# Performance work log

Hardware: AMD Instinct MI355X
Metric: run time of the kernel (lower is better)

## Reference

```python
import jax, jax.numpy as jnp
import numpy as np

B, D, M, C = 8192, 2048, 8, 1000

def setup_inputs() -> dict:
    key = jax.random.key(0)
    k1, k2, k3, k4, k5 = jax.random.split(key, 5)
    scale = 1.0 / np.sqrt(D)
    return {
        "x": jax.random.normal(k1, (B, D), dtype=jnp.float32),
        "model_weights": jax.random.normal(k2, (M, D, C), dtype=jnp.float32) * scale,
        "model_bias": jax.random.normal(k3, (M, C), dtype=jnp.float32) * 0.01,
        "resnet_weight": jax.random.normal(k4, (D, M * C), dtype=jnp.float32) * scale,
        "resnet_bias": jax.random.normal(k5, (M * C,), dtype=jnp.float32) * 0.01,
    }

def reference(x, model_weights, model_bias, resnet_weight, resnet_bias):
    # Per-submodel logits: [B, M, C]
    outputs = jnp.einsum("bd,mdc->bmc", x, model_weights) + model_bias[None, :, :]
    # Fusion weights from the weighting network: [B, M, C]
    w = (x @ resnet_weight + resnet_bias).reshape(x.shape[0], model_weights.shape[0], model_weights.shape[2])
    # Fused weighted sum over models (replaces the triple Python loop): [B, C]
    result = jnp.sum(outputs * w, axis=1)
    return result
```

## Files before the change

### kernel.cpp

```cpp
#include <hip/hip_runtime.h>
#include <hip/hip_bf16.h>
#include <stdint.h>

#define BDIM 8192
#define DDIM 2048
#define MDIM 8
#define CDIM 1000
#define CPAD 1024
#define NPAD 8192

typedef __attribute__((ext_vector_type(8))) short bf16x8;
typedef __attribute__((ext_vector_type(4))) float f32x4;

__device__ __forceinline__ unsigned short f2bf(float f) {
    union { float f; unsigned u; } v; v.f = f;
    unsigned r = v.u + 0x7fffu + ((v.u >> 16) & 1u);
    return (unsigned short)(r >> 16);
}

__device__ __forceinline__ void gl_lds16(const void* g, void* l) {
    __builtin_amdgcn_global_load_lds(
        (const __attribute__((address_space(1))) void*)g,
        (__attribute__((address_space(3))) void*)l,
        16, 0, 0);
}

__global__ void cast_x_kernel(const float4* __restrict__ x, ushort* __restrict__ xb) {
    int i = blockIdx.x * blockDim.x + threadIdx.x;
    float4 v = x[i];
    ushort4 o;
    o.x = f2bf(v.x); o.y = f2bf(v.y); o.z = f2bf(v.z); o.w = f2bf(v.w);
    *(ushort4*)&xb[(size_t)i * 4] = o;
}

__global__ void prep_w(const float* __restrict__ MW, ushort* __restrict__ wb) {
    __shared__ float tile[32][33];
    int m  = blockIdx.z;
    int c0 = blockIdx.x * 32;
    int d0 = blockIdx.y * 32;
    int tx = threadIdx.x, ty = threadIdx.y;
    const float* src = MW + (size_t)m * DDIM * CDIM;
#pragma unroll
    for (int i = 0; i < 4; i++) {
        int d = d0 + ty + i * 8;
        int c = c0 + tx;
        tile[ty + i * 8][tx] = (c < CDIM) ? src[(size_t)d * CDIM + c] : 0.f;
    }
    __syncthreads();
#pragma unroll
    for (int i = 0; i < 4; i++) {
        int c = c0 + ty + i * 8;
        int d = d0 + tx;
        wb[(size_t)(c * 8 + m) * DDIM + d] = f2bf(tile[tx][ty + i * 8]);
    }
}

__global__ void prep_r(const float* __restrict__ R, ushort* __restrict__ rb) {
    __shared__ float tile[32][33];
    int m  = blockIdx.z;
    int c0 = blockIdx.x * 32;
    int d0 = blockIdx.y * 32;
    int tx = threadIdx.x, ty = threadIdx.y;
#pragma unroll
    for (int i = 0; i < 4; i++) {
        int d = d0 + ty + i * 8;
        int c = c0 + tx;
        tile[ty + i * 8][tx] = (c < CDIM) ? R[(size_t)d * (MDIM * CDIM) + m * CDIM + c] : 0.f;
    }
    __syncthreads();
#pragma unroll
    for (int i = 0; i < 4; i++) {
        int c = c0 + ty + i * 8;
        int d = d0 + tx;
        rb[(size_t)(c * 8 + m) * DDIM + d] = f2bf(tile[tx][ty + i * 8]);
    }
}

__global__ void prep_bias(const float* __restrict__ mb, const float* __restrict__ rbv,
                          float* __restrict__ mb2, float* __restrict__ rb2) {
    int n = blockIdx.x * 256 + threadIdx.x;
    int c = n >> 3, m = n & 7;
    mb2[n] = (c < CDIM) ? mb[m * CDIM + c] : 0.f;
    rb2[n] = (c < CDIM) ? rbv[m * CDIM + c] : 0.f;
}

#define BM 256
#define BN 128
#define BK 32
#define NT (DDIM / BK)


#define STAGE_A(G, L) do {                                                     \
    _Pragma("unroll")                                                          \
    for (int it_ = 0; it_ < 2; ++it_) {                                        \
        int ci_ = it_ * 512 + tid;                                             \
        int r_ = ci_ >> 2, cc_ = ci_ & 3;                                      \
        gl_lds16((G) + (size_t)r_ * DDIM + (size_t)((cc_ ^ ((r_ >> 1) & 3)) << 3), \
                 (L) + (size_t)(it_ * 512 + wbase) * 8);                       \
    }                                                                          \
} while (0)

#define STAGE_B(G, L) do {                                                     \
    int r_ = tid >> 2, cc_ = tid & 3;                                          \
    gl_lds16((G) + (size_t)r_ * DDIM + (size_t)((cc_ ^ ((r_ >> 1) & 3)) << 3), \
             (L) + (size_t)wbase * 8);                                         \
} while (0)

#define LDA4(AC, H) do {                                                       \
    _Pragma("unroll")                                                          \
    for (int i_ = 0; i_ < 4; i_++) {                                           \
        int row_ = wm * 128 + (H) * 64 + i_ * 16 + (lane & 15);                \
        int cc_ = lane >> 4;                                                   \
        af[i_] = *(const bf16x8*)&(AC)[row_ * BK + ((cc_ ^ ((row_ >> 1) & 3)) << 3)]; \
    }                                                                          \
} while (0)

#define LDB2(BS, BF) do {                                                      \
    _Pragma("unroll")                                                          \
    for (int j_ = 0; j_ < 2; j_++) {                                           \
        int row_ = wn * 32 + j_ * 16 + (lane & 15);                            \
        int cc_ = lane >> 4;                                                   \
        BF[j_] = *(const bf16x8*)&(BS)[row_ * BK + ((cc_ ^ ((row_ >> 1) & 3)) << 3)]; \
    }                                                                          \
} while (0)

#define MM16(H) do {                                                           \
    __builtin_amdgcn_s_setprio(1);                                             \
    _Pragma("unroll")                                                          \
    for (int i_ = 0; i_ < 4; i_++)                                             \
    _Pragma("unroll")                                                          \
    for (int j_ = 0; j_ < 2; j_++) {                                           \
        acc1[(H) * 4 + i_][j_] = __builtin_amdgcn_mfma_f32_16x16x32_bf16(      \
            af[i_], bf1[j_], acc1[(H) * 4 + i_][j_], 0, 0, 0);                 \
        acc2[(H) * 4 + i_][j_] = __builtin_amdgcn_mfma_f32_16x16x32_bf16(      \
            af[i_], bf2[j_], acc2[(H) * 4 + i_][j_], 0, 0, 0);                 \
    }                                                                          \
    __builtin_amdgcn_s_setprio(0);                                             \
} while (0)

#define FENCE() asm volatile("" ::: "memory")
#define BARRIER() do { FENCE(); __builtin_amdgcn_s_barrier(); FENCE(); } while (0)
#define WAITV(N) asm volatile("s_waitcnt vmcnt(" #N ")" ::: "memory")

__global__ __launch_bounds__(512, 2) void gemm_fused(
    const ushort* __restrict__ xb, const ushort* __restrict__ wb,
    const ushort* __restrict__ rb,
    const float* __restrict__ mb2, const float* __restrict__ rb2,
    float* __restrict__ out) {
    __shared__ ushort As[2][BM * BK];
    __shared__ ushort B1s[2][BN * BK];
    __shared__ ushort B2s[2][BN * BK];

    int tid   = threadIdx.x;
    int lane  = tid & 63;
    int wid   = tid >> 6;
    int wm    = wid >> 2;
    int wn    = wid & 3;
    int wbase = tid & ~63;

    int wg = blockIdx.x;
    int wgs = (wg & 7) * 256 + (wg >> 3);
    int tile_m = wgs >> 6;
    int tile_n = wgs & 63;
    int brow = tile_m * BM;
    int bn0  = tile_n * BN;

    const ushort* xg  = xb + (size_t)brow * DDIM;
    const ushort* w1g = wb + (size_t)bn0 * DDIM;
    const ushort* w2g = rb + (size_t)bn0 * DDIM;

    f32x4 acc1[8][2] = {};
    f32x4 acc2[8][2] = {};
    bf16x8 af[4], bf1[2], bf2[2];

    STAGE_A(xg,        As[0]);
    STAGE_B(w1g,       B1s[0]);
    STAGE_B(w2g,       B2s[0]);
    STAGE_A(xg + BK,   As[1]);
    WAITV(2);
    BARRIER();

#pragma unroll 2
    for (int t = 0; t < NT; ++t) {
        int buf = t & 1;
        ushort* Ac  = As[buf];
        ushort* B1c = B1s[buf];
        ushort* B2c = B2s[buf];
        ushort* B1n = B1s[buf ^ 1];
        ushort* B2n = B2s[buf ^ 1];
        const int kn  = (t + 1) * BK;
        const int kn2 = (t + 2) * BK;

        LDA4(Ac, 0);
        LDB2(B1c, bf1);
        LDB2(B2c, bf2);
        STAGE_B(w1g + kn, B1n);
        STAGE_B(w2g + kn, B2n);
        BARRIER();
        MM16(0);
        BARRIER();

        LDA4(Ac, 1);
        STAGE_A(xg + kn2, Ac);
        BARRIER();
        MM16(1);
        WAITV(2);
        BARRIER();
    }
    WAITV(0);

#pragma unroll
    for (int j = 0; j < 2; j++) {
        int np = bn0 + wn * 32 + j * 16 + (lane & 15);
        float bb1 = mb2[np];
        float bb2 = rb2[np];
        int c = tile_n * 16 + wn * 4 + j * 2 + ((lane >> 3) & 1);
#pragma unroll
        for (int rf = 0; rf < 8; rf++) {
#pragma unroll
            for (int r = 0; r < 4; r++) {
                float p = (acc1[rf][j][r] + bb1) * (acc2[rf][j][r] + bb2);
                p += __shfl_xor(p, 1);
                p += __shfl_xor(p, 2);
                p += __shfl_xor(p, 4);
                if ((lane & 7) == 0 && c < CDIM) {
                    int row = brow + wm * 128 + rf * 16 + ((lane >> 4) << 2) + r;
                    out[(size_t)row * CDIM + c] = p;
                }
            }
        }
    }
}

extern "C" void kernel_launch(void* const* d_in, const int* in_sizes, int n_in,
                              void* d_out, int out_size, void* d_ws, size_t ws_size,
                              hipStream_t stream) {
    const float* x   = (const float*)d_in[0];
    const float* mw  = (const float*)d_in[1];
    const float* mb  = (const float*)d_in[2];
    const float* rw  = (const float*)d_in[3];
    const float* rbv = (const float*)d_in[4];
    float* out = (float*)d_out;

    char* ws = (char*)d_ws;
    ushort* xb  = (ushort*)ws;
    ushort* wb  = (ushort*)(ws + (size_t)33554432);
    ushort* rb  = (ushort*)(ws + (size_t)67108864);
    float*  mb2 = (float*)(ws + (size_t)100663296);
    float*  rb2 = (float*)(ws + (size_t)100696064);

    cast_x_kernel<<<BDIM * DDIM / (256 * 4), 256, 0, stream>>>((const float4*)x, xb);
    prep_w<<<dim3(CPAD / 32, DDIM / 32, MDIM), dim3(32, 8), 0, stream>>>(mw, wb);
    prep_r<<<dim3(CPAD / 32, DDIM / 32, MDIM), dim3(32, 8), 0, stream>>>(rw, rb);
    prep_bias<<<NPAD / 256, 256, 0, stream>>>(mb, rbv, mb2, rb2);

    gemm_fused<<<dim3((BDIM / BM) * (NPAD / BN)), 512, 0, stream>>>(xb, wb, rb, mb2, rb2, out);
}
```

Before: 641.7 us.

## Shrink GEMM tile to 128x128 with 4 waves and triple-buffered A staging

Halves the row tile to 128 and the workgroup to 256 threads (4 waves, each owning all 128 rows and a 32-column slice). A is now staged into a 3-deep LDS ring and B into double buffers, all prefetched two K-steps ahead, so every stage load is issued after the current buffer's reads. This aims for deeper prefetch and more, smaller workgroups for better latency hiding. In exchange each tile reuses x and the weights less, which raises total global and LDS traffic per FLOP, and the loop is no longer unrolled.

```diff
diff --git a/kernel.cpp b/kernel.cpp
--- a/kernel.cpp
+++ b/kernel.cpp
@@ -84,34 +84,27 @@
     rb2[n] = (c < CDIM) ? rbv[m * CDIM + c] : 0.f;
 }
 
-#define BM 256
+#define BM 128
 #define BN 128
 #define BK 32
 #define NT (DDIM / BK)
 
-
-#define STAGE_A(G, L) do {                                                     \
+#define STAGE(G, L) do {                                                       \
     _Pragma("unroll")                                                          \
     for (int it_ = 0; it_ < 2; ++it_) {                                        \
-        int ci_ = it_ * 512 + tid;                                             \
+        int ci_ = it_ * 256 + tid;                                             \
         int r_ = ci_ >> 2, cc_ = ci_ & 3;                                      \
         gl_lds16((G) + (size_t)r_ * DDIM + (size_t)((cc_ ^ ((r_ >> 1) & 3)) << 3), \
-                 (L) + (size_t)(it_ * 512 + wbase) * 8);                       \
-    }                                                                          \
-} while (0)
-
-#define STAGE_B(G, L) do {                                                     \
-    int r_ = tid >> 2, cc_ = tid & 3;                                          \
-    gl_lds16((G) + (size_t)r_ * DDIM + (size_t)((cc_ ^ ((r_ >> 1) & 3)) << 3), \
-             (L) + (size_t)wbase * 8);                                         \
-} while (0)
-
-#define LDA4(AC, H) do {                                                       \
+                 (L) + (size_t)(it_ * 256 + wbase) * 8);                       \
+    }                                                                          \
+} while (0)
+
+#define LDA4(AC, I0) do {                                                      \
     _Pragma("unroll")                                                          \
     for (int i_ = 0; i_ < 4; i_++) {                                           \
-        int row_ = wm * 128 + (H) * 64 + i_ * 16 + (lane & 15);                \
+        int row_ = ((I0) + i_) * 16 + (lane & 15);                             \
         int cc_ = lane >> 4;                                                   \
-        af[i_] = *(const bf16x8*)&(AC)[row_ * BK + ((cc_ ^ ((row_ >> 1) & 3)) << 3)]; \
+        af[(I0) + i_] = *(const bf16x8*)&(AC)[row_ * BK + ((cc_ ^ ((row_ >> 1) & 3)) << 3)]; \
     }                                                                          \
 } while (0)
 
@@ -124,16 +117,16 @@
     }                                                                          \
 } while (0)
 
-#define MM16(H) do {                                                           \
+#define MM16(I0) do {                                                          \
     __builtin_amdgcn_s_setprio(1);                                             \
     _Pragma("unroll")                                                          \
     for (int i_ = 0; i_ < 4; i_++)                                             \
     _Pragma("unroll")                                                          \
     for (int j_ = 0; j_ < 2; j_++) {                                           \
-        acc1[(H) * 4 + i_][j_] = __builtin_amdgcn_mfma_f32_16x16x32_bf16(      \
-            af[i_], bf1[j_], acc1[(H) * 4 + i_][j_], 0, 0, 0);                 \
-        acc2[(H) * 4 + i_][j_] = __builtin_amdgcn_mfma_f32_16x16x32_bf16(      \
-            af[i_], bf2[j_], acc2[(H) * 4 + i_][j_], 0, 0, 0);                 \
+        acc1[(I0) + i_][j_] = __builtin_amdgcn_mfma_f32_16x16x32_bf16(         \
+            af[(I0) + i_], bf1[j_], acc1[(I0) + i_][j_], 0, 0, 0);             \
+        acc2[(I0) + i_][j_] = __builtin_amdgcn_mfma_f32_16x16x32_bf16(         \
+            af[(I0) + i_], bf2[j_], acc2[(I0) + i_][j_], 0, 0, 0);             \
     }                                                                          \
     __builtin_amdgcn_s_setprio(0);                                             \
 } while (0)
@@ -142,24 +135,22 @@
 #define BARRIER() do { FENCE(); __builtin_amdgcn_s_barrier(); FENCE(); } while (0)
 #define WAITV(N) asm volatile("s_waitcnt vmcnt(" #N ")" ::: "memory")
 
-__global__ __launch_bounds__(512, 2) void gemm_fused(
+__global__ __launch_bounds__(256, 2) void gemm_fused(
     const ushort* __restrict__ xb, const ushort* __restrict__ wb,
     const ushort* __restrict__ rb,
     const float* __restrict__ mb2, const float* __restrict__ rb2,
     float* __restrict__ out) {
-    __shared__ ushort As[2][BM * BK];
+    __shared__ ushort As[3][BM * BK];
     __shared__ ushort B1s[2][BN * BK];
     __shared__ ushort B2s[2][BN * BK];
 
     int tid   = threadIdx.x;
     int lane  = tid & 63;
-    int wid   = tid >> 6;
-    int wm    = wid >> 2;
-    int wn    = wid & 3;
+    int wn    = tid >> 6;
     int wbase = tid & ~63;
 
     int wg = blockIdx.x;
-    int wgs = (wg & 7) * 256 + (wg >> 3);
+    int wgs = (wg & 7) * 512 + (wg >> 3);
     int tile_m = wgs >> 6;
     int tile_n = wgs & 63;
     int brow = tile_m * BM;
@@ -171,40 +162,35 @@
 
     f32x4 acc1[8][2] = {};
     f32x4 acc2[8][2] = {};
-    bf16x8 af[4], bf1[2], bf2[2];
-
-    STAGE_A(xg,        As[0]);
-    STAGE_B(w1g,       B1s[0]);
-    STAGE_B(w2g,       B2s[0]);
-    STAGE_A(xg + BK,   As[1]);
-    WAITV(2);
+    bf16x8 af[8], bf1[2], bf2[2];
+
+    STAGE(xg,        As[0]);  STAGE(w1g,        B1s[0]);  STAGE(w2g,        B2s[0]);
+    STAGE(xg + BK,   As[1]);  STAGE(w1g + BK,   B1s[1]);  STAGE(w2g + BK,   B2s[1]);
+    WAITV(6);
     BARRIER();
 
-#pragma unroll 2
+#pragma unroll 1
     for (int t = 0; t < NT; ++t) {
-        int buf = t & 1;
-        ushort* Ac  = As[buf];
-        ushort* B1c = B1s[buf];
-        ushort* B2c = B2s[buf];
-        ushort* B1n = B1s[buf ^ 1];
-        ushort* B2n = B2s[buf ^ 1];
-        const int kn  = (t + 1) * BK;
+        ushort* Ac  = As[t % 3];
+        ushort* An2 = As[(t + 2) % 3];
+        ushort* B1c = B1s[t & 1];
+        ushort* B2c = B2s[t & 1];
         const int kn2 = (t + 2) * BK;
 
         LDA4(Ac, 0);
         LDB2(B1c, bf1);
         LDB2(B2c, bf2);
-        STAGE_B(w1g + kn, B1n);
-        STAGE_B(w2g + kn, B2n);
         BARRIER();
         MM16(0);
         BARRIER();
 
-        LDA4(Ac, 1);
-        STAGE_A(xg + kn2, Ac);
-        BARRIER();
-        MM16(1);
-        WAITV(2);
+        LDA4(Ac, 4);
+        STAGE(xg + kn2,  An2);
+        STAGE(w1g + kn2, B1s[t & 1]);
+        STAGE(w2g + kn2, B2s[t & 1]);
+        BARRIER();
+        MM16(4);
+        WAITV(6);
         BARRIER();
     }
     WAITV(0);
@@ -224,7 +210,7 @@
                 p += __shfl_xor(p, 2);
                 p += __shfl_xor(p, 4);
                 if ((lane & 7) == 0 && c < CDIM) {
-                    int row = brow + wm * 128 + rf * 16 + ((lane >> 4) << 2) + r;
+                    int row = brow + rf * 16 + ((lane >> 4) << 2) + r;
                     out[(size_t)row * CDIM + c] = p;
                 }
             }
@@ -254,5 +240,5 @@
     prep_r<<<dim3(CPAD / 32, DDIM / 32, MDIM), dim3(32, 8), 0, stream>>>(rw, rb);
     prep_bias<<<NPAD / 256, 256, 0, stream>>>(mb, rbv, mb2, rb2);
 
-    gemm_fused<<<dim3((BDIM / BM) * (NPAD / BN)), 512, 0, stream>>>(xb, wb, rb, mb2, rb2, out);
-}
+    gemm_fused<<<dim3((BDIM / BM) * (NPAD / BN)), 256, 0, stream>>>(xb, wb, rb, mb2, rb2, out);
+}
```

Result: slower. 730.9 us (+13.9%).
